# Kernel optimization log

Hardware: AMD Instinct MI355X
Metric: run time of the kernel (lower is better)

Reference implementation:

```python
import jax, jax.numpy as jnp
import numpy as np

H = 256  # hidden_size


def setup_inputs() -> dict:
    key = jax.random.key(0)
    k1, k2, k3 = jax.random.split(key, 3)
    N, L, V, Emb = 128, 2048, 32000, 256
    X = jax.random.randint(k1, (N, L), 0, V, dtype=jnp.int64)
    E = jax.random.normal(k2, (V, Emb), dtype=jnp.float32) * 0.02
    W_w = jax.random.normal(k3, (4 * H, H + Emb), dtype=jnp.float32) * (1.0 / np.sqrt(H + Emb))
    W_b = jnp.zeros((4 * H,), dtype=jnp.float32)
    return {"X": X, "E": E, "W_w": W_w, "W_b": W_b}


def reference(X, E, W_w, W_b):
    # X: (N, L) int token ids
    N, L = X.shape
    Xe = E[X]                      # (N, L, Emb) embedded sequence
    Xe_t = jnp.swapaxes(Xe, 0, 1)  # (L, N, Emb) scan over time

    def step(carry, x_t):
        H_t, C_t = carry
        hx = jnp.concatenate([H_t, x_t], axis=1)           # (N, H+Emb)
        G = hx @ W_w.T + W_b                               # (N, 4H)
        F_g = jax.nn.sigmoid(G[:, :H])
        # NOTE: original code computes I = sigmoid(G[:, H:2H]) but never uses it
        O_g = jax.nn.sigmoid(G[:, 2 * H:3 * H])
        H_tmp = jnp.tanh(G[:, 3 * H:4 * H])
        # Faithful to source: C_t = F*C + O*H_tmp (uses O, not I)
        C_new = F_g * C_t + O_g * H_tmp
        H_new = O_g * jnp.tanh(C_new)
        return (H_new, C_new), None

    init = (jnp.zeros((N, H), Xe.dtype), jnp.zeros((N, H), Xe.dtype))
    (H_last, _), _ = jax.lax.scan(step, init, Xe_t)
    return H_last
```

## Files before the change

### kernel.cpp

```cpp
#include <hip/hip_runtime.h>
#include <hip/hip_bf16.h>

#define N_B   128
#define L_SEQ 2048
#define H_DIM 256
#define EMB   256
#define G3    768
#define G4    1024
#define WROW  512
#define V_SZ  32000


typedef unsigned short ushort_t;
typedef unsigned int   uint_t;

using f32x4  = __attribute__((ext_vector_type(4))) float;
using bf16x8 = __attribute__((ext_vector_type(8))) short;
using h2_t   = __attribute__((ext_vector_type(2))) _Float16;
using ushort4_t = __attribute__((ext_vector_type(4))) ushort_t;
using u32x4  = __attribute__((ext_vector_type(4))) uint_t;

__device__ __forceinline__ float bf2f(ushort_t u) {
  union { uint_t u; float f; } x; x.u = ((uint_t)u) << 16; return x.f;
}
__device__ __forceinline__ ushort_t f2bf(float f) {
  union { float f; uint_t u; } x; x.f = f;
  return (ushort_t)((x.u + 0x7fffu + ((x.u >> 16) & 1u)) >> 16);
}
__device__ __forceinline__ float rcp_f(float x) {
#if __has_builtin(__builtin_amdgcn_rcpf)
  return __builtin_amdgcn_rcpf(x);
#else
  return 1.0f / x;
#endif
}
__device__ __forceinline__ float clampf(float x, float lo, float hi) {
  return fminf(fmaxf(x, lo), hi);
}
__device__ __forceinline__ float sigmoid_f(float x) {
  x = clampf(x, -30.f, 30.f);
  return rcp_f(1.0f + __expf(-x));
}
__device__ __forceinline__ float tanh_f(float x) {
  x = clampf(x, -15.f, 15.f);
  float e = __expf(-2.0f * x);
  return (1.0f - e) * rcp_f(1.0f + e);
}
__device__ __forceinline__ float fdot2_f(h2_t a, h2_t b, float c) {
#if __has_builtin(__builtin_amdgcn_fdot2)
  return __builtin_amdgcn_fdot2(a, b, c, false);
#else
  return c + (float)a.x * (float)b.x + (float)a.y * (float)b.y;
#endif
}
__device__ __forceinline__ uint_t lane_bcast(uint_t v, int l) {
#if __has_builtin(__builtin_amdgcn_readlane)
  return (uint_t)__builtin_amdgcn_readlane((int)v, l);
#else
  return (uint_t)__shfl((int)v, l, 64);
#endif
}
__device__ __forceinline__ h2_t bfpair_to_h2(uint_t u) {
  union { uint_t u; float f; } lo, hi;
  lo.u = u << 16;
  hi.u = u & 0xffff0000u;
  h2_t r; r.x = (_Float16)lo.f; r.y = (_Float16)hi.f; return r;
}

__device__ __forceinline__ int gmap(int g) { return (g < 256) ? g : g + 256; }

__global__ void dtype_probe(const uint_t* __restrict__ Ed,
                            const uint_t* __restrict__ Xd,
                            const uint_t* __restrict__ Wd,
                            uint_t* __restrict__ flags) {
  if (threadIdx.x != 0 || blockIdx.x != 0) return;
  int saneE = 0, saneW = 0;
  for (int i = 0; i < 256; ++i) {
    uint_t le = Ed[i] & 0xffffu, ee = (le >> 7) & 0xffu;
    if (ee == 0u || (ee >= 90u && ee <= 126u)) saneE++;
    uint_t lw = Wd[i] & 0xffffu, ew = (lw >> 7) & 0xffu;
    if (ew == 0u || (ew >= 90u && ew <= 126u)) saneW++;
  }
  uint_t nz = 0u;
  for (int i = 0; i < 128; ++i) nz |= Xd[2 * i + 1];
  flags[0] = (saneE < 192) ? 1u : 0u;
  flags[1] = (nz == 0u) ? 1u : 0u;
  flags[2] = (saneW < 192) ? 1u : 0u;
}

__global__ __launch_bounds__(256) void eg_gemm(const void* __restrict__ Ein,
                                               const void* __restrict__ Wwin,
                                               const void* __restrict__ Wbin,
                                               _Float16* __restrict__ Eg,
                                               const uint_t* __restrict__ flags) {
  __shared__ __align__(16) ushort_t At[16][264];
  const int tid = threadIdx.x;
  const int v0  = blockIdx.x * 16;
  const uint_t ef32 = flags[0];
  const uint_t wf32 = flags[2];

  if (!ef32) {
    const ushort_t* E = (const ushort_t*)Ein;
#pragma unroll
    for (int i = 0; i < 2; ++i) {
      int idx = tid + i * 256;
      int row = idx >> 5, seg = idx & 31;
      const uint4* src = (const uint4*)(E + (size_t)(v0 + row) * EMB + seg * 8);
      *(uint4*)&At[row][seg * 8] = *src;
    }
  } else {
    const float* Ef = (const float*)Ein;
#pragma unroll
    for (int i = 0; i < 4; ++i) {
      int idx = tid + i * 256;
      int row = idx >> 6, seg = idx & 63;
      float4 v = *(const float4*)(Ef + (size_t)(v0 + row) * EMB + seg * 4);
      ushort4_t s;
      s.x = f2bf(v.x); s.y = f2bf(v.y); s.z = f2bf(v.z); s.w = f2bf(v.w);
      *(ushort4_t*)&At[row][seg * 4] = s;
    }
  }
  __syncthreads();

  const int lane = tid & 63, wv = tid >> 6;
  const int m = lane & 15, q = lane >> 4;

  f32x4 acc[12];
#pragma unroll
  for (int nt = 0; nt < 12; ++nt) acc[nt] = f32x4{0.f, 0.f, 0.f, 0.f};

  if (!wf32) {
    const ushort_t* Ww = (const ushort_t*)Wwin;
#pragma unroll
    for (int kt = 0; kt < 8; ++kt) {
      bf16x8 a = *(const bf16x8*)&At[m][kt * 32 + q * 8];
#pragma unroll
      for (int nt = 0; nt < 12; ++nt) {
        int g  = wv * 192 + nt * 16 + m;
        int gr = gmap(g);
        const bf16x8* bp =
            (const bf16x8*)(Ww + (size_t)gr * WROW + EMB + kt * 32 + q * 8);
        acc[nt] = __builtin_amdgcn_mfma_f32_16x16x32_bf16(a, *bp, acc[nt], 0, 0, 0);
      }
    }
  } else {
    const float* Wf = (const float*)Wwin;
#pragma unroll
    for (int kt = 0; kt < 8; ++kt) {
      bf16x8 a = *(const bf16x8*)&At[m][kt * 32 + q * 8];
#pragma unroll
      for (int nt = 0; nt < 12; ++nt) {
        int g  = wv * 192 + nt * 16 + m;
        int gr = gmap(g);
        const float* wp = Wf + (size_t)gr * WROW + EMB + kt * 32 + q * 8;
        float4 w0 = *(const float4*)(wp);
        float4 w1 = *(const float4*)(wp + 4);
        bf16x8 b;
        b[0] = (short)f2bf(w0.x); b[1] = (short)f2bf(w0.y);
        b[2] = (short)f2bf(w0.z); b[3] = (short)f2bf(w0.w);
        b[4] = (short)f2bf(w1.x); b[5] = (short)f2bf(w1.y);
        b[6] = (short)f2bf(w1.z); b[7] = (short)f2bf(w1.w);
        acc[nt] = __builtin_amdgcn_mfma_f32_16x16x32_bf16(a, b, acc[nt], 0, 0, 0);
      }
    }
  }

#pragma unroll
  for (int nt = 0; nt < 12; ++nt) {
    int g  = wv * 192 + nt * 16 + m;
    int gr = gmap(g);
    float bias = wf32 ? ((const float*)Wbin)[gr] : bf2f(((const ushort_t*)Wbin)[gr]);
#pragma unroll
    for (int j = 0; j < 4; ++j) {
      int v = v0 + q * 4 + j;
      Eg[(size_t)v * G3 + g] = (_Float16)(acc[nt][j] + bias);
    }
  }
}

__global__
__attribute__((amdgpu_flat_work_group_size(1024, 1024), amdgpu_waves_per_eu(4, 4)))
void lstm_rec(const int* __restrict__ Xi,
              const void* __restrict__ Wwin,
              const _Float16* __restrict__ Eg,
              float* __restrict__ out,
              const uint_t* __restrict__ flags) {
  __shared__ uint_t hbuf[2][128];
  __shared__ float  pbuf[3][G3];
  const int tid  = threadIdx.x;
  const int lane = tid & 63;
  const int q4   = tid >> 8;
  const int j    = tid & 255;
  const int n    = blockIdx.x;
  const uint_t wf32 = flags[2];
  const uint_t x64  = flags[1];

  uint_t w[96];
  if (!wf32) {
    const ushort_t* Wb16 = (const ushort_t*)Wwin;
#pragma unroll
    for (int G = 0; G < 3; ++G) {
      const int row = (G == 0) ? j : ((G == 1) ? 512 + j : 768 + j);
      const u32x4* src = (const u32x4*)(Wb16 + (size_t)row * WROW + q4 * 64);
#pragma unroll
      for (int i = 0; i < 8; ++i) {
        u32x4 v = src[i];
#pragma unroll
        for (int cdw = 0; cdw < 4; ++cdw)
          w[G * 32 + i * 4 + cdw] = __builtin_bit_cast(uint_t, bfpair_to_h2(v[cdw]));
      }
    }
  } else {
    const float* Wf = (const float*)Wwin;
#pragma unroll
    for (int G = 0; G < 3; ++G) {
      const int row = (G == 0) ? j : ((G == 1) ? 512 + j : 768 + j);
      const float* src = Wf + (size_t)row * WROW + q4 * 64;
#pragma unroll
      for (int dd = 0; dd < 32; ++dd) {
        float2 v = *(const float2*)(src + 2 * dd);
        h2_t p; p.x = (_Float16)v.x; p.y = (_Float16)v.y;
        w[G * 32 + dd] = __builtin_bit_cast(uint_t, p);
      }
    }
  }
#pragma unroll
  for (int dd = 0; dd < 96; ++dd) asm volatile("" : "+v"(w[dd]));

  if (tid < 128) hbuf[0][tid] = 0u;

  float c = 0.f, hlast = 0.f;
  const size_t xbase = (size_t)n * L_SEQ;

  float pxF = 0.f, pxO = 0.f, pxT = 0.f;
  if (q4 == 0) {
    int tok0 = x64 ? Xi[xbase * 2] : Xi[xbase];
    if ((uint_t)tok0 >= (uint_t)V_SZ) tok0 = 0;
    const _Float16* e = Eg + (size_t)tok0 * G3 + j;
    pxF = (float)e[0]; pxO = (float)e[256]; pxT = (float)e[512];
  }

  int cur = 0;
  for (int t = 0; t < L_SEQ; ++t) {
    __syncthreads();

    const uint_t hv = hbuf[cur][q4 * 32 + (lane & 31)];

    float nF = 0.f, nO = 0.f, nT = 0.f;
    if (q4 == 0) {
      int tp = (t + 1 < L_SEQ) ? (t + 1) : (L_SEQ - 1);
      int tok = x64 ? Xi[(xbase + tp) * 2] : Xi[xbase + tp];
      if ((uint_t)tok >= (uint_t)V_SZ) tok = 0;
      const _Float16* e = Eg + (size_t)tok * G3 + j;
      nF = (float)e[0]; nO = (float)e[256]; nT = (float)e[512];
    }

    float aF0 = 0.f, aO0 = 0.f, aT0 = 0.f;
    float aF1 = 0.f, aO1 = 0.f, aT1 = 0.f;
#pragma unroll
    for (int d = 0; d < 32; ++d) {
      h2_t hh = __builtin_bit_cast(h2_t, lane_bcast(hv, d));
      h2_t wf = __builtin_bit_cast(h2_t, w[d]);
      h2_t wo = __builtin_bit_cast(h2_t, w[32 + d]);
      h2_t wt = __builtin_bit_cast(h2_t, w[64 + d]);
      if (d & 1) {
        aF1 = fdot2_f(wf, hh, aF1);
        aO1 = fdot2_f(wo, hh, aO1);
        aT1 = fdot2_f(wt, hh, aT1);
      } else {
        aF0 = fdot2_f(wf, hh, aF0);
        aO0 = fdot2_f(wo, hh, aO0);
        aT0 = fdot2_f(wt, hh, aT0);
      }
    }
    float aF = aF0 + aF1, aO = aO0 + aO1, aT = aT0 + aT1;

    if (q4 != 0) {
      pbuf[q4 - 1][j]       = aF;
      pbuf[q4 - 1][256 + j] = aO;
      pbuf[q4 - 1][512 + j] = aT;
    }
    __syncthreads();

    if (q4 == 0) {
      aF += pbuf[0][j]       + pbuf[1][j]       + pbuf[2][j]       + pxF;
      aO += pbuf[0][256 + j] + pbuf[1][256 + j] + pbuf[2][256 + j] + pxO;
      aT += pbuf[0][512 + j] + pbuf[1][512 + j] + pbuf[2][512 + j] + pxT;
      float Fg = sigmoid_f(aF);
      float Og = sigmoid_f(aO);
      float Tg = tanh_f(aT);
      c = Fg * c + Og * Tg;
      float hv2 = Og * tanh_f(c);
      hlast = hv2;
      ((_Float16*)hbuf[cur ^ 1])[j] = (_Float16)hv2;
      pxF = nF; pxO = nO; pxT = nT;
    }
    cur ^= 1;
  }

  if (q4 == 0) out[(size_t)n * H_DIM + j] = hlast;
}

extern "C" void kernel_launch(void* const* d_in, const int* in_sizes, int n_in,
                              void* d_out, int out_size, void* d_ws, size_t ws_size,
                              hipStream_t stream) {
  const void* X  = d_in[0];
  const void* E  = d_in[1];
  const void* Ww = d_in[2];
  const void* Wb = d_in[3];
  for (int i = 0; i < n_in && i < 4; ++i) {
    switch (in_sizes[i]) {
      case N_B * L_SEQ: X  = d_in[i]; break;
      case V_SZ * EMB:  E  = d_in[i]; break;
      case G4 * WROW:   Ww = d_in[i]; break;
      case G4:          Wb = d_in[i]; break;
      default: break;
    }
  }
  float* out = (float*)d_out;

  uint_t*   flags = (uint_t*)d_ws;
  _Float16* Eg    = (_Float16*)((char*)d_ws + 256);

  dtype_probe<<<dim3(1), dim3(64), 0, stream>>>(
      (const uint_t*)E, (const uint_t*)X, (const uint_t*)Ww, flags);
  eg_gemm<<<dim3(V_SZ / 16), dim3(256), 0, stream>>>(E, Ww, Wb, Eg, flags);
  lstm_rec<<<dim3(N_B), dim3(1024), 0, stream>>>((const int*)X, Ww, Eg, out, flags);
}
```

Before: 3.003 ms.

## Compute recurrent matvec with MFMA f16 and register-resident weights in 512-thread blocks

Replaces the per-lane fdot2 dot products and readlane broadcasts of h with MFMA 16x16x32 f16 instructions. Weights are held as A fragments in registers, and h is loaded from LDS as the B operand. Each wave computes 96 gate rows over the full K=256, which removes the cross-quarter partial-sum reduction through LDS. The block shrinks to 512 threads. The trade-off is that only one output column of each MFMA is used, so most of the matrix throughput is wasted on the broadcast h.

```diff
diff --git a/kernel.cpp b/kernel.cpp
--- a/kernel.cpp
+++ b/kernel.cpp
@@ -17,6 +17,7 @@
 using f32x4  = __attribute__((ext_vector_type(4))) float;
 using bf16x8 = __attribute__((ext_vector_type(8))) short;
 using h2_t   = __attribute__((ext_vector_type(2))) _Float16;
+using f16x8  = __attribute__((ext_vector_type(8))) _Float16;
 using ushort4_t = __attribute__((ext_vector_type(4))) ushort_t;
 using u32x4  = __attribute__((ext_vector_type(4))) uint_t;
 
@@ -46,20 +47,6 @@
   float e = __expf(-2.0f * x);
   return (1.0f - e) * rcp_f(1.0f + e);
 }
-__device__ __forceinline__ float fdot2_f(h2_t a, h2_t b, float c) {
-#if __has_builtin(__builtin_amdgcn_fdot2)
-  return __builtin_amdgcn_fdot2(a, b, c, false);
-#else
-  return c + (float)a.x * (float)b.x + (float)a.y * (float)b.y;
-#endif
-}
-__device__ __forceinline__ uint_t lane_bcast(uint_t v, int l) {
-#if __has_builtin(__builtin_amdgcn_readlane)
-  return (uint_t)__builtin_amdgcn_readlane((int)v, l);
-#else
-  return (uint_t)__shfl((int)v, l, 64);
-#endif
-}
 __device__ __forceinline__ h2_t bfpair_to_h2(uint_t u) {
   union { uint_t u; float f; } lo, hi;
   lo.u = u << 16;
@@ -68,6 +55,10 @@
 }
 
 __device__ __forceinline__ int gmap(int g) { return (g < 256) ? g : g + 256; }
+
+#define FENCE_V8(A) asm volatile("" :                                         \
+  "+v"((A)[0]), "+v"((A)[1]), "+v"((A)[2]), "+v"((A)[3]),                     \
+  "+v"((A)[4]), "+v"((A)[5]), "+v"((A)[6]), "+v"((A)[7]))
 
 __global__ void dtype_probe(const uint_t* __restrict__ Ed,
                             const uint_t* __restrict__ Xd,
@@ -178,65 +169,80 @@
   }
 }
 
-__global__
-__attribute__((amdgpu_flat_work_group_size(1024, 1024), amdgpu_waves_per_eu(4, 4)))
-void lstm_rec(const int* __restrict__ Xi,
-              const void* __restrict__ Wwin,
-              const _Float16* __restrict__ Eg,
-              float* __restrict__ out,
-              const uint_t* __restrict__ flags) {
-  __shared__ uint_t hbuf[2][128];
-  __shared__ float  pbuf[3][G3];
+__global__ __launch_bounds__(512)
+void lstm_rec_mfma(const int* __restrict__ Xi,
+                   const void* __restrict__ Wwin,
+                   const _Float16* __restrict__ Eg,
+                   float* __restrict__ out,
+                   const uint_t* __restrict__ flags) {
+  __shared__ __align__(16) _Float16 hbuf[2][256];
+  __shared__ __align__(16) float    Gbuf[G3];
   const int tid  = threadIdx.x;
   const int lane = tid & 63;
-  const int q4   = tid >> 8;
-  const int j    = tid & 255;
+  const int w    = tid >> 6;
+  const int q    = lane >> 4;
+  const int rr   = lane & 15;
   const int n    = blockIdx.x;
   const uint_t wf32 = flags[2];
   const uint_t x64  = flags[1];
 
-  uint_t w[96];
+  u32x4 wAq[48];
   if (!wf32) {
     const ushort_t* Wb16 = (const ushort_t*)Wwin;
 #pragma unroll
-    for (int G = 0; G < 3; ++G) {
-      const int row = (G == 0) ? j : ((G == 1) ? 512 + j : 768 + j);
-      const u32x4* src = (const u32x4*)(Wb16 + (size_t)row * WROW + q4 * 64);
-#pragma unroll
-      for (int i = 0; i < 8; ++i) {
-        u32x4 v = src[i];
-#pragma unroll
-        for (int cdw = 0; cdw < 4; ++cdw)
-          w[G * 32 + i * 4 + cdw] = __builtin_bit_cast(uint_t, bfpair_to_h2(v[cdw]));
+    for (int m = 0; m < 6; ++m) {
+      const int grow = (w * 6 + m) * 16 + rr;
+      const int wr   = gmap(grow);
+      const ushort_t* rp = Wb16 + (size_t)wr * WROW + q * 8;
+#pragma unroll
+      for (int kt = 0; kt < 8; ++kt) {
+        u32x4 v = *(const u32x4*)(rp + kt * 32);
+        u32x4 t;
+#pragma unroll
+        for (int cc = 0; cc < 4; ++cc)
+          t[cc] = __builtin_bit_cast(uint_t, bfpair_to_h2(v[cc]));
+        wAq[m * 8 + kt] = t;
       }
     }
   } else {
     const float* Wf = (const float*)Wwin;
 #pragma unroll
-    for (int G = 0; G < 3; ++G) {
-      const int row = (G == 0) ? j : ((G == 1) ? 512 + j : 768 + j);
-      const float* src = Wf + (size_t)row * WROW + q4 * 64;
-#pragma unroll
-      for (int dd = 0; dd < 32; ++dd) {
-        float2 v = *(const float2*)(src + 2 * dd);
-        h2_t p; p.x = (_Float16)v.x; p.y = (_Float16)v.y;
-        w[G * 32 + dd] = __builtin_bit_cast(uint_t, p);
-      }
-    }
-  }
-#pragma unroll
-  for (int dd = 0; dd < 96; ++dd) asm volatile("" : "+v"(w[dd]));
-
-  if (tid < 128) hbuf[0][tid] = 0u;
+    for (int m = 0; m < 6; ++m) {
+      const int grow = (w * 6 + m) * 16 + rr;
+      const int wr   = gmap(grow);
+      const float* rp = Wf + (size_t)wr * WROW + q * 8;
+#pragma unroll
+      for (int kt = 0; kt < 8; ++kt) {
+        const float* pp = rp + kt * 32;
+        float4 a = *(const float4*)(pp);
+        float4 b = *(const float4*)(pp + 4);
+        h2_t p0, p1, p2, p3;
+        p0.x = (_Float16)a.x; p0.y = (_Float16)a.y;
+        p1.x = (_Float16)a.z; p1.y = (_Float16)a.w;
+        p2.x = (_Float16)b.x; p2.y = (_Float16)b.y;
+        p3.x = (_Float16)b.z; p3.y = (_Float16)b.w;
+        u32x4 t;
+        t[0] = __builtin_bit_cast(uint_t, p0);
+        t[1] = __builtin_bit_cast(uint_t, p1);
+        t[2] = __builtin_bit_cast(uint_t, p2);
+        t[3] = __builtin_bit_cast(uint_t, p3);
+        wAq[m * 8 + kt] = t;
+      }
+    }
+  }
+  FENCE_V8(wAq);      FENCE_V8(wAq + 8);  FENCE_V8(wAq + 16);
+  FENCE_V8(wAq + 24); FENCE_V8(wAq + 32); FENCE_V8(wAq + 40);
+
+  if (tid < 256) hbuf[0][tid] = (_Float16)0.f;
 
   float c = 0.f, hlast = 0.f;
   const size_t xbase = (size_t)n * L_SEQ;
 
   float pxF = 0.f, pxO = 0.f, pxT = 0.f;
-  if (q4 == 0) {
+  if (tid < 256) {
     int tok0 = x64 ? Xi[xbase * 2] : Xi[xbase];
     if ((uint_t)tok0 >= (uint_t)V_SZ) tok0 = 0;
-    const _Float16* e = Eg + (size_t)tok0 * G3 + j;
+    const _Float16* e = Eg + (size_t)tok0 * G3 + tid;
     pxF = (float)e[0]; pxO = (float)e[256]; pxT = (float)e[512];
   }
 
@@ -244,61 +250,57 @@
   for (int t = 0; t < L_SEQ; ++t) {
     __syncthreads();
 
-    const uint_t hv = hbuf[cur][q4 * 32 + (lane & 31)];
+    u32x4 bfq[8];
+#pragma unroll
+    for (int kt = 0; kt < 8; ++kt)
+      bfq[kt] = *(const u32x4*)&hbuf[cur][kt * 32 + q * 8];
 
     float nF = 0.f, nO = 0.f, nT = 0.f;
-    if (q4 == 0) {
+    if (tid < 256) {
       int tp = (t + 1 < L_SEQ) ? (t + 1) : (L_SEQ - 1);
       int tok = x64 ? Xi[(xbase + tp) * 2] : Xi[xbase + tp];
       if ((uint_t)tok >= (uint_t)V_SZ) tok = 0;
-      const _Float16* e = Eg + (size_t)tok * G3 + j;
+      const _Float16* e = Eg + (size_t)tok * G3 + tid;
       nF = (float)e[0]; nO = (float)e[256]; nT = (float)e[512];
     }
 
-    float aF0 = 0.f, aO0 = 0.f, aT0 = 0.f;
-    float aF1 = 0.f, aO1 = 0.f, aT1 = 0.f;
-#pragma unroll
-    for (int d = 0; d < 32; ++d) {
-      h2_t hh = __builtin_bit_cast(h2_t, lane_bcast(hv, d));
-      h2_t wf = __builtin_bit_cast(h2_t, w[d]);
-      h2_t wo = __builtin_bit_cast(h2_t, w[32 + d]);
-      h2_t wt = __builtin_bit_cast(h2_t, w[64 + d]);
-      if (d & 1) {
-        aF1 = fdot2_f(wf, hh, aF1);
-        aO1 = fdot2_f(wo, hh, aO1);
-        aT1 = fdot2_f(wt, hh, aT1);
-      } else {
-        aF0 = fdot2_f(wf, hh, aF0);
-        aO0 = fdot2_f(wo, hh, aO0);
-        aT0 = fdot2_f(wt, hh, aT0);
-      }
-    }
-    float aF = aF0 + aF1, aO = aO0 + aO1, aT = aT0 + aT1;
-
-    if (q4 != 0) {
-      pbuf[q4 - 1][j]       = aF;
-      pbuf[q4 - 1][256 + j] = aO;
-      pbuf[q4 - 1][512 + j] = aT;
+    f32x4 acc[6];
+#pragma unroll
+    for (int m = 0; m < 6; ++m) acc[m] = f32x4{0.f, 0.f, 0.f, 0.f};
+#pragma unroll
+    for (int kt = 0; kt < 8; ++kt) {
+      f16x8 b = __builtin_bit_cast(f16x8, bfq[kt]);
+#pragma unroll
+      for (int m = 0; m < 6; ++m) {
+        f16x8 a = __builtin_bit_cast(f16x8, wAq[m * 8 + kt]);
+        acc[m] = __builtin_amdgcn_mfma_f32_16x16x32_f16(a, b, acc[m], 0, 0, 0);
+      }
+    }
+
+    if (rr == 0) {
+#pragma unroll
+      for (int m = 0; m < 6; ++m)
+        *(f32x4*)&Gbuf[(w * 6 + m) * 16 + q * 4] = acc[m];
     }
     __syncthreads();
 
-    if (q4 == 0) {
-      aF += pbuf[0][j]       + pbuf[1][j]       + pbuf[2][j]       + pxF;
-      aO += pbuf[0][256 + j] + pbuf[1][256 + j] + pbuf[2][256 + j] + pxO;
-      aT += pbuf[0][512 + j] + pbuf[1][512 + j] + pbuf[2][512 + j] + pxT;
+    if (tid < 256) {
+      float aF = Gbuf[tid]       + pxF;
+      float aO = Gbuf[256 + tid] + pxO;
+      float aT = Gbuf[512 + tid] + pxT;
       float Fg = sigmoid_f(aF);
       float Og = sigmoid_f(aO);
       float Tg = tanh_f(aT);
       c = Fg * c + Og * Tg;
       float hv2 = Og * tanh_f(c);
       hlast = hv2;
-      ((_Float16*)hbuf[cur ^ 1])[j] = (_Float16)hv2;
+      hbuf[cur ^ 1][tid] = (_Float16)hv2;
       pxF = nF; pxO = nO; pxT = nT;
     }
     cur ^= 1;
   }
 
-  if (q4 == 0) out[(size_t)n * H_DIM + j] = hlast;
+  if (tid < 256) out[(size_t)n * H_DIM + tid] = hlast;
 }
 
 extern "C" void kernel_launch(void* const* d_in, const int* in_sizes, int n_in,
@@ -325,5 +327,6 @@
   dtype_probe<<<dim3(1), dim3(64), 0, stream>>>(
       (const uint_t*)E, (const uint_t*)X, (const uint_t*)Ww, flags);
   eg_gemm<<<dim3(V_SZ / 16), dim3(256), 0, stream>>>(E, Ww, Wb, Eg, flags);
-  lstm_rec<<<dim3(N_B), dim3(1024), 0, stream>>>((const int*)X, Ww, Eg, out, flags);
-}
+  lstm_rec_mfma<<<dim3(N_B), dim3(512), 0, stream>>>(
+      (const int*)X, Ww, Eg, out, flags);
+}
```

Result: slower. 3.360 ms (+11.9%).
